# Kernel tuning notes

Measured on AMD Instinct MI355X. Metric: run time of the kernel, lower is better.

## Reference

```python
import jax, jax.numpy as jnp
import numpy as np

K = 16            # max_num_neighbors
RADIUS = 8.0      # interaction_radius
RBF = 128         # rbf_size == hidden_channels
HIDDEN = 128


def setup_inputs() -> dict:
    key = jax.random.key(0)
    k1, _ = jax.random.split(key)
    num_graphs = 64
    n_per_graph = 512
    # 3D coords; randn*3 gives realistic spread so radius mask is nontrivial
    pos = jax.random.normal(k1, (num_graphs * n_per_graph, 3), dtype=jnp.float32) * 3.0
    bias = jnp.zeros((HIDDEN,), dtype=jnp.float32)  # Parameter(zeros), requires_grad=False
    return {"pos": pos, "bias": bias, "num_graphs": num_graphs}


def reference(pos, bias, num_graphs):
    N = pos.shape[0]
    n = N // num_graphs                       # nodes per graph (uniform batch)
    p = pos.reshape(num_graphs, n, 3)
    # pairwise squared distances per graph: [B, n, n]
    d2 = jnp.sum((p[:, :, None, :] - p[:, None, :, :]) ** 2, axis=-1)
    # kNN with self-loop (loop=True): K+1 smallest distances per target node
    neg_d2, idx = jax.lax.top_k(-d2, K + 1)   # [B, n, K+1]
    d = jnp.sqrt(jnp.maximum(-neg_d2, 1e-12))
    # global edge_index: row = source (neighbor), col = target node
    graph_off = (jnp.arange(num_graphs) * n)[:, None, None]
    src = (idx + graph_off).reshape(-1)
    dst = jnp.broadcast_to(jnp.arange(n)[None, :, None] + graph_off,
                           (num_graphs, n, K + 1)).reshape(-1)
    edge_index = jnp.stack([src, dst])        # [2, B*n*(K+1)]
    dist = d.reshape(-1)
    # radius mask (original filters edges; we keep fixed shape and zero invalid rows)
    mask = dist <= RADIUS
    # Gaussian RBF distance embedding
    offsets = jnp.linspace(0.0, RADIUS, RBF, dtype=pos.dtype)
    coeff = -0.5 / (offsets[1] - offsets[0]) ** 2
    emb = jnp.exp(coeff * (dist[:, None] - offsets[None, :]) ** 2)  # [E, RBF]
    # forward: edge_repr = zeros + process_weight(dist); out = act(edge_repr + bias), act='none'
    edge_repr = emb + bias
    edge_repr = jnp.where(mask[:, None], edge_repr, 0.0)
    return edge_index, edge_repr, mask
```

## Files before the change

### kernel.cpp

```cpp
#include <hip/hip_runtime.h>
#include <math.h>

#define NPG   512
#define KK    17
#define RBFN  128
#define TPB   128
#define WPB   2
#define TGT_PER_WAVE 8
#define TGT_PER_BLK  16
#define BPG   (NPG / TGT_PER_BLK)
#define NCH   2
#define TPC   4
#define NSC   16
#define CPS   32
#define SITERS 34
#define LSTR  20

#define WAVE_SYNC()                                      \
  do {                                                   \
    asm volatile("s_waitcnt lgkmcnt(0)" ::: "memory");   \
    __builtin_amdgcn_sched_barrier(0);                   \
  } while (0)

__device__ __forceinline__ unsigned gmin16(unsigned v) {
  unsigned t;
  t = (unsigned)__builtin_amdgcn_ds_swizzle((int)v, 0x041F); v = v < t ? v : t;
  t = (unsigned)__builtin_amdgcn_ds_swizzle((int)v, 0x081F); v = v < t ? v : t;
  t = (unsigned)__builtin_amdgcn_ds_swizzle((int)v, 0x101F); v = v < t ? v : t;
  t = (unsigned)__builtin_amdgcn_ds_swizzle((int)v, 0x201F); v = v < t ? v : t;
  return v;
}

__global__ __launch_bounds__(TPB, 4) void fused_kernel(
    const float* __restrict__ pos, const float* __restrict__ bias,
    float* __restrict__ out, int E) {
  __shared__ float4 ps[NPG];
  __shared__ float  bs[RBFN];
  __shared__ __align__(16) unsigned LA[WPB][64][LSTR];
  __shared__ float  dd[WPB][TPC][KK];

  const int g = blockIdx.x / BPG;
  const int p = blockIdx.x % BPG;
  const float* gp = pos + (size_t)g * NPG * 3;
  for (int i = threadIdx.x; i < NPG; i += TPB)
    ps[i] = make_float4(gp[3 * i], gp[3 * i + 1], gp[3 * i + 2], 0.0f);
  bs[threadIdx.x] = bias[threadIdx.x];
  __syncthreads();

  const int w = threadIdx.x >> 6;
  const int lane = threadIdx.x & 63;
  const int tl = lane >> 4;
  const int q = lane & 15;

  float* __restrict__ srcp = out;
  float* __restrict__ dstp = out + (size_t)E;
  float* __restrict__ repr = out + 2 * (size_t)E;
  float* __restrict__ mskp = out + 130 * (size_t)E;

  const float step = 8.0f / 127.0f;
  const float coeff = -0.5f / (step * step);
  const int sc0 = (lane & 31) << 2;
  const float4 bv = *reinterpret_cast<const float4*>(bs + sc0);
  const float o0 = (float)(sc0 + 0) * step, o1 = (float)(sc0 + 1) * step,
              o2 = (float)(sc0 + 2) * step, o3 = (float)(sc0 + 3) * step;

  const int tbase = p * TGT_PER_BLK + w * TGT_PER_WAVE;
  const int goff = g * NPG;

  unsigned b0, b1, b2, b3, b4, b5, b6, b7, b8, b9, b10, b11, b12, b13, b14,
      b15, b16;
  float px, py, pz;

  auto scan_init = [&](int c) {
    const float4 me = ps[tbase + c * TPC + tl];
    px = me.x; py = me.y; pz = me.z;
    b0 = b1 = b2 = b3 = b4 = b5 = b6 = b7 = b8 = b9 = b10 = b11 = b12 = b13 =
        b14 = b15 = b16 = 0xFFFFFFFFu;
  };

#define CE(B)                                    \
  {                                              \
    const unsigned mn_ = key < (B) ? key : (B);  \
    const unsigned mx_ = key < (B) ? (B) : key;  \
    (B) = mn_;                                   \
    key = mx_;                                   \
  }
  auto scan_iter = [&](int jj) {
    const int j = (jj << 4) | q;
    const float4 c4 = ps[j];
    const float dx = __fsub_rn(px, c4.x);
    const float dy = __fsub_rn(py, c4.y);
    const float dz = __fsub_rn(pz, c4.z);
    const float d2 = __fadd_rn(
        __fadd_rn(__fmul_rn(dx, dx), __fmul_rn(dy, dy)), __fmul_rn(dz, dz));
    unsigned key = (__float_as_uint(d2) & 0xFFFFFE00u) | (unsigned)j;
    CE(b0) CE(b1) CE(b2) CE(b3) CE(b4) CE(b5) CE(b6) CE(b7) CE(b8)
    CE(b9) CE(b10) CE(b11) CE(b12) CE(b13) CE(b14) CE(b15) CE(b16)
  };
#undef CE

  auto merge_emit = [&](int c) {
    {
      uint4* Lv = reinterpret_cast<uint4*>(&LA[w][lane][0]);
      Lv[0] = make_uint4(b0, b1, b2, b3);
      Lv[1] = make_uint4(b4, b5, b6, b7);
      Lv[2] = make_uint4(b8, b9, b10, b11);
      Lv[3] = make_uint4(b12, b13, b14, b15);
      LA[w][lane][16] = b16;
      LA[w][lane][17] = 0xFFFFFFFFu;
    }
    WAVE_SYNC();
    const unsigned* L = &LA[w][lane][0];
    int i = 0;
    unsigned h = L[0];
    unsigned cap0 = 0, cap1 = 0;
#pragma unroll
    for (int k = 0; k < KK; ++k) {
      const unsigned mn = gmin16(h);
      if (k < 16) cap0 = (q == k) ? mn : cap0;
      else        cap1 = (q == 0) ? mn : cap1;
      const bool adv = (h == mn);
      i += adv;
      const unsigned nxt = L[i];
      h = adv ? nxt : h;
    }
    const int t = tbase + c * TPC + tl;
    const int node = goff + t;
    const size_t ebase = (size_t)node * KK;
    {
      const int jv = (int)(cap0 & 511u);
      const float4 cj = ps[jv];
      const float dx = __fsub_rn(px, cj.x);
      const float dy = __fsub_rn(py, cj.y);
      const float dz = __fsub_rn(pz, cj.z);
      const float d2 = __fadd_rn(
          __fadd_rn(__fmul_rn(dx, dx), __fmul_rn(dy, dy)), __fmul_rn(dz, dz));
      const float dv = __fsqrt_rn(fmaxf(d2, 1e-12f));
      srcp[ebase + q] = (float)(jv + goff);
      dstp[ebase + q] = (float)node;
      mskp[ebase + q] = (dv <= 8.0f) ? 1.0f : 0.0f;
      dd[w][tl][q] = dv;
    }
    if (q == 0) {
      const int jv = (int)(cap1 & 511u);
      const float4 cj = ps[jv];
      const float dx = __fsub_rn(px, cj.x);
      const float dy = __fsub_rn(py, cj.y);
      const float dz = __fsub_rn(pz, cj.z);
      const float d2 = __fadd_rn(
          __fadd_rn(__fmul_rn(dx, dx), __fmul_rn(dy, dy)), __fmul_rn(dz, dz));
      const float dv = __fsqrt_rn(fmaxf(d2, 1e-12f));
      srcp[ebase + 16] = (float)(jv + goff);
      dstp[ebase + 16] = (float)node;
      mskp[ebase + 16] = (dv <= 8.0f) ? 1.0f : 0.0f;
      dd[w][tl][16] = dv;
    }
  };

  auto store_iter = [&](float4* __restrict__ rb, int it) {
    const int gi = (it << 6) + lane;
    const int el = gi >> 5;
    const int tp = (el * 3856) >> 16;
    const int kk = el - tp * 17;
    const float dist = dd[w][tp][kk];
    const bool ok = dist <= 8.0f;
    float4 o;
    { const float d_ = __fsub_rn(dist, o0); o.x = ok ? (__expf(coeff * d_ * d_) + bv.x) : 0.0f; }
    { const float d_ = __fsub_rn(dist, o1); o.y = ok ? (__expf(coeff * d_ * d_) + bv.y) : 0.0f; }
    { const float d_ = __fsub_rn(dist, o2); o.z = ok ? (__expf(coeff * d_ * d_) + bv.z) : 0.0f; }
    { const float d_ = __fsub_rn(dist, o3); o.w = ok ? (__expf(coeff * d_ * d_) + bv.w) : 0.0f; }
    rb[gi] = o;
  };

  scan_init(0);
  for (int jj = 0; jj < CPS; ++jj) scan_iter(jj);
  merge_emit(0);
  WAVE_SYNC();

  scan_init(1);
  {
    float4* rb = reinterpret_cast<float4*>(repr) +
                 (size_t)(goff + tbase) * (KK * RBFN / 4);
#pragma unroll 2
    for (int it = 0; it < SITERS; ++it) {
      if (it < CPS) scan_iter(it);
      store_iter(rb, it);
    }
  }
  merge_emit(1);
  WAVE_SYNC();

  {
    float4* rb = reinterpret_cast<float4*>(repr) +
                 (size_t)(goff + tbase + TPC) * (KK * RBFN / 4);
#pragma unroll 2
    for (int it = 0; it < SITERS; ++it) store_iter(rb, it);
  }
}

extern "C" void kernel_launch(void* const* d_in, const int* in_sizes, int n_in,
                              void* d_out, int out_size, void* d_ws, size_t ws_size,
                              hipStream_t stream) {
  const float* pos = (const float*)d_in[0];
  const float* bias = (const float*)d_in[1];
  (void)n_in; (void)d_ws; (void)ws_size; (void)out_size;

  const int N = in_sizes[0] / 3;
  const int B = N / NPG;
  const int E = N * KK;
  float* out = (float*)d_out;

  fused_kernel<<<B * BPG, TPB, 0, stream>>>(pos, bias, out, E);
}
```

Before: 55.59 us.

## Split kNN scan across 32 lanes and fuse RBF stores into merge loop

```diff
diff --git a/kernel.cpp b/kernel.cpp
--- a/kernel.cpp
+++ b/kernel.cpp
@@ -6,14 +6,13 @@
 #define RBFN  128
 #define TPB   128
 #define WPB   2
-#define TGT_PER_WAVE 8
-#define TGT_PER_BLK  16
+#define TPC   2
+#define NSC   32
+#define CPS   16
+#define NCH   4
+#define TGT_PER_WAVE (TPC * NCH)
+#define TGT_PER_BLK  (WPB * TGT_PER_WAVE)
 #define BPG   (NPG / TGT_PER_BLK)
-#define NCH   2
-#define TPC   4
-#define NSC   16
-#define CPS   32
-#define SITERS 34
 #define LSTR  20
 
 #define WAVE_SYNC()                                      \
@@ -22,12 +21,13 @@
     __builtin_amdgcn_sched_barrier(0);                   \
   } while (0)
 
-__device__ __forceinline__ unsigned gmin16(unsigned v) {
+__device__ __forceinline__ unsigned gmin32(unsigned v) {
   unsigned t;
   t = (unsigned)__builtin_amdgcn_ds_swizzle((int)v, 0x041F); v = v < t ? v : t;
   t = (unsigned)__builtin_amdgcn_ds_swizzle((int)v, 0x081F); v = v < t ? v : t;
   t = (unsigned)__builtin_amdgcn_ds_swizzle((int)v, 0x101F); v = v < t ? v : t;
   t = (unsigned)__builtin_amdgcn_ds_swizzle((int)v, 0x201F); v = v < t ? v : t;
+  t = (unsigned)__builtin_amdgcn_ds_swizzle((int)v, 0x401F); v = v < t ? v : t;
   return v;
 }
 
@@ -35,48 +35,39 @@
     const float* __restrict__ pos, const float* __restrict__ bias,
     float* __restrict__ out, int E) {
   __shared__ float4 ps[NPG];
-  __shared__ float  bs[RBFN];
   __shared__ __align__(16) unsigned LA[WPB][64][LSTR];
-  __shared__ float  dd[WPB][TPC][KK];
 
   const int g = blockIdx.x / BPG;
   const int p = blockIdx.x % BPG;
   const float* gp = pos + (size_t)g * NPG * 3;
   for (int i = threadIdx.x; i < NPG; i += TPB)
     ps[i] = make_float4(gp[3 * i], gp[3 * i + 1], gp[3 * i + 2], 0.0f);
-  bs[threadIdx.x] = bias[threadIdx.x];
   __syncthreads();
 
   const int w = threadIdx.x >> 6;
   const int lane = threadIdx.x & 63;
-  const int tl = lane >> 4;
-  const int q = lane & 15;
+  const int tl = lane >> 5;
+  const int q = lane & 31;
 
   float* __restrict__ srcp = out;
   float* __restrict__ dstp = out + (size_t)E;
   float* __restrict__ repr = out + 2 * (size_t)E;
   float* __restrict__ mskp = out + 130 * (size_t)E;
+  float4* __restrict__ repr4 = reinterpret_cast<float4*>(repr);
 
   const float step = 8.0f / 127.0f;
   const float coeff = -0.5f / (step * step);
-  const int sc0 = (lane & 31) << 2;
-  const float4 bv = *reinterpret_cast<const float4*>(bs + sc0);
-  const float o0 = (float)(sc0 + 0) * step, o1 = (float)(sc0 + 1) * step,
-              o2 = (float)(sc0 + 2) * step, o3 = (float)(sc0 + 3) * step;
+  const int c0 = q << 2;
+  const float4 bv = *reinterpret_cast<const float4*>(bias + c0);
+  const float o0 = (float)(c0 + 0) * step, o1 = (float)(c0 + 1) * step,
+              o2 = (float)(c0 + 2) * step, o3 = (float)(c0 + 3) * step;
 
   const int tbase = p * TGT_PER_BLK + w * TGT_PER_WAVE;
   const int goff = g * NPG;
 
   unsigned b0, b1, b2, b3, b4, b5, b6, b7, b8, b9, b10, b11, b12, b13, b14,
-      b15, b16;
+      b15;
   float px, py, pz;
-
-  auto scan_init = [&](int c) {
-    const float4 me = ps[tbase + c * TPC + tl];
-    px = me.x; py = me.y; pz = me.z;
-    b0 = b1 = b2 = b3 = b4 = b5 = b6 = b7 = b8 = b9 = b10 = b11 = b12 = b13 =
-        b14 = b15 = b16 = 0xFFFFFFFFu;
-  };
 
 #define CE(B)                                    \
   {                                              \
@@ -85,50 +76,72 @@
     (B) = mn_;                                   \
     key = mx_;                                   \
   }
-  auto scan_iter = [&](int jj) {
-    const int j = (jj << 4) | q;
-    const float4 c4 = ps[j];
-    const float dx = __fsub_rn(px, c4.x);
-    const float dy = __fsub_rn(py, c4.y);
-    const float dz = __fsub_rn(pz, c4.z);
-    const float d2 = __fadd_rn(
-        __fadd_rn(__fmul_rn(dx, dx), __fmul_rn(dy, dy)), __fmul_rn(dz, dz));
-    unsigned key = (__float_as_uint(d2) & 0xFFFFFE00u) | (unsigned)j;
-    CE(b0) CE(b1) CE(b2) CE(b3) CE(b4) CE(b5) CE(b6) CE(b7) CE(b8)
-    CE(b9) CE(b10) CE(b11) CE(b12) CE(b13) CE(b14) CE(b15) CE(b16)
-  };
-#undef CE
 
-  auto merge_emit = [&](int c) {
+  for (int c = 0; c < NCH; ++c) {
+    const int t = tbase + c * TPC + tl;
+    {
+      const float4 me = ps[t];
+      px = me.x; py = me.y; pz = me.z;
+    }
+    b0 = b1 = b2 = b3 = b4 = b5 = b6 = b7 = b8 = b9 = b10 = b11 = b12 = b13 =
+        b14 = b15 = 0xFFFFFFFFu;
+#pragma unroll 4
+    for (int jj = 0; jj < CPS; ++jj) {
+      const int j = (jj << 5) | q;
+      const float4 c4 = ps[j];
+      const float dx = __fsub_rn(px, c4.x);
+      const float dy = __fsub_rn(py, c4.y);
+      const float dz = __fsub_rn(pz, c4.z);
+      const float d2 = __fadd_rn(
+          __fadd_rn(__fmul_rn(dx, dx), __fmul_rn(dy, dy)), __fmul_rn(dz, dz));
+      unsigned key = (__float_as_uint(d2) & 0xFFFFFE00u) | (unsigned)j;
+      CE(b0) CE(b1) CE(b2) CE(b3) CE(b4) CE(b5) CE(b6) CE(b7) CE(b8)
+      CE(b9) CE(b10) CE(b11) CE(b12) CE(b13) CE(b14) CE(b15)
+    }
+
     {
       uint4* Lv = reinterpret_cast<uint4*>(&LA[w][lane][0]);
       Lv[0] = make_uint4(b0, b1, b2, b3);
       Lv[1] = make_uint4(b4, b5, b6, b7);
       Lv[2] = make_uint4(b8, b9, b10, b11);
       Lv[3] = make_uint4(b12, b13, b14, b15);
-      LA[w][lane][16] = b16;
-      LA[w][lane][17] = 0xFFFFFFFFu;
+      LA[w][lane][16] = 0xFFFFFFFFu;
     }
     WAVE_SYNC();
+
+    const int node = goff + t;
+    const size_t ebase = (size_t)node * KK;
+    float4* __restrict__ rb = repr4 + (size_t)node * (KK * RBFN / 4);
     const unsigned* L = &LA[w][lane][0];
     int i = 0;
     unsigned h = L[0];
-    unsigned cap0 = 0, cap1 = 0;
+    unsigned cap = 0;
 #pragma unroll
     for (int k = 0; k < KK; ++k) {
-      const unsigned mn = gmin16(h);
-      if (k < 16) cap0 = (q == k) ? mn : cap0;
-      else        cap1 = (q == 0) ? mn : cap1;
+      const unsigned mn = gmin32(h);
+      cap = (q == k) ? mn : cap;
+      const int jv = (int)(mn & 511u);
+      const float4 cj = ps[jv];
+      const float dx = __fsub_rn(px, cj.x);
+      const float dy = __fsub_rn(py, cj.y);
+      const float dz = __fsub_rn(pz, cj.z);
+      const float d2 = __fadd_rn(
+          __fadd_rn(__fmul_rn(dx, dx), __fmul_rn(dy, dy)), __fmul_rn(dz, dz));
+      const float dv = __fsqrt_rn(fmaxf(d2, 1e-12f));
+      const float okf = (dv <= 8.0f) ? 1.0f : 0.0f;
+      float4 o;
+      { const float d_ = __fsub_rn(dv, o0); o.x = (__expf(coeff * d_ * d_) + bv.x) * okf; }
+      { const float d_ = __fsub_rn(dv, o1); o.y = (__expf(coeff * d_ * d_) + bv.y) * okf; }
+      { const float d_ = __fsub_rn(dv, o2); o.z = (__expf(coeff * d_ * d_) + bv.z) * okf; }
+      { const float d_ = __fsub_rn(dv, o3); o.w = (__expf(coeff * d_ * d_) + bv.w) * okf; }
+      rb[k * 32 + q] = o;
       const bool adv = (h == mn);
       i += adv;
       const unsigned nxt = L[i];
       h = adv ? nxt : h;
     }
-    const int t = tbase + c * TPC + tl;
-    const int node = goff + t;
-    const size_t ebase = (size_t)node * KK;
-    {
-      const int jv = (int)(cap0 & 511u);
+    if (q < KK) {
+      const int jv = (int)(cap & 511u);
       const float4 cj = ps[jv];
       const float dx = __fsub_rn(px, cj.x);
       const float dy = __fsub_rn(py, cj.y);
@@ -139,63 +152,10 @@
       srcp[ebase + q] = (float)(jv + goff);
       dstp[ebase + q] = (float)node;
       mskp[ebase + q] = (dv <= 8.0f) ? 1.0f : 0.0f;
-      dd[w][tl][q] = dv;
     }
-    if (q == 0) {
-      const int jv = (int)(cap1 & 511u);
-      const float4 cj = ps[jv];
-      const float dx = __fsub_rn(px, cj.x);
-      const float dy = __fsub_rn(py, cj.y);
-      const float dz = __fsub_rn(pz, cj.z);
-      const float d2 = __fadd_rn(
-          __fadd_rn(__fmul_rn(dx, dx), __fmul_rn(dy, dy)), __fmul_rn(dz, dz));
-      const float dv = __fsqrt_rn(fmaxf(d2, 1e-12f));
-      srcp[ebase + 16] = (float)(jv + goff);
-      dstp[ebase + 16] = (float)node;
-      mskp[ebase + 16] = (dv <= 8.0f) ? 1.0f : 0.0f;
-      dd[w][tl][16] = dv;
-    }
-  };
-
-  auto store_iter = [&](float4* __restrict__ rb, int it) {
-    const int gi = (it << 6) + lane;
-    const int el = gi >> 5;
-    const int tp = (el * 3856) >> 16;
-    const int kk = el - tp * 17;
-    const float dist = dd[w][tp][kk];
-    const bool ok = dist <= 8.0f;
-    float4 o;
-    { const float d_ = __fsub_rn(dist, o0); o.x = ok ? (__expf(coeff * d_ * d_) + bv.x) : 0.0f; }
-    { const float d_ = __fsub_rn(dist, o1); o.y = ok ? (__expf(coeff * d_ * d_) + bv.y) : 0.0f; }
-    { const float d_ = __fsub_rn(dist, o2); o.z = ok ? (__expf(coeff * d_ * d_) + bv.z) : 0.0f; }
-    { const float d_ = __fsub_rn(dist, o3); o.w = ok ? (__expf(coeff * d_ * d_) + bv.w) : 0.0f; }
-    rb[gi] = o;
-  };
-
-  scan_init(0);
-  for (int jj = 0; jj < CPS; ++jj) scan_iter(jj);
-  merge_emit(0);
-  WAVE_SYNC();
-
-  scan_init(1);
-  {
-    float4* rb = reinterpret_cast<float4*>(repr) +
-                 (size_t)(goff + tbase) * (KK * RBFN / 4);
-#pragma unroll 2
-    for (int it = 0; it < SITERS; ++it) {
-      if (it < CPS) scan_iter(it);
-      store_iter(rb, it);
-    }
+    WAVE_SYNC();
   }
-  merge_emit(1);
-  WAVE_SYNC();
-
-  {
-    float4* rb = reinterpret_cast<float4*>(repr) +
-                 (size_t)(goff + tbase + TPC) * (KK * RBFN / 4);
-#pragma unroll 2
-    for (int it = 0; it < SITERS; ++it) store_iter(rb, it);
-  }
+#undef CE
 }
 
 extern "C" void kernel_launch(void* const* d_in, const int* in_sizes, int n_in,
```

After: 56.69 us. Within noise of the previous version (+2.0%).
